# Performance work log

Measured on AMD Instinct MI355X. Metric: run time of the kernel, lower is better.

## Reference

```python
import jax, jax.numpy as jnp
import numpy as np

B, T, CH, V, E, L = 64, 1024, 256, 32000, 64, 128  # batch, enc_len, channel, vocab, emb_dim, latent_dims


def setup_inputs() -> dict:
    key = jax.random.key(0)
    ks = jax.random.split(key, 13)
    s = 0.05  # weight init scale
    return {
        "prev_cont_vec": jax.random.normal(ks[0], (B, CH), jnp.float32),
        "F": jax.random.normal(ks[1], (B, T, CH), jnp.float32),
        "prev_char": jax.random.normal(ks[2], (B, V), jnp.float32),
        "state_h": jax.random.normal(ks[3], (B, L), jnp.float32),
        "state_c": jax.random.normal(ks[4], (B, L), jnp.float32),
        # learned parameters (all Dense layers use_bias=False)
        "Wc": jax.random.normal(ks[5], (V, E), jnp.float32) * s,
        "Wct1": jax.random.normal(ks[6], (CH, E), jnp.float32) * s,
        "Wo": jax.random.normal(ks[7], (L, V), jnp.float32) * s,
        "Wct2": jax.random.normal(ks[8], (CH, V), jnp.float32) * s,
        "lstm_kernel": jax.random.normal(ks[9], (E, 4 * L), jnp.float32) * s,
        "lstm_recurrent": jax.random.normal(ks[10], (L, 4 * L), jnp.float32) * s,
        "W_h": jax.random.normal(ks[11], (L, CH), jnp.float32) * s,
        "V_attn": jax.random.normal(ks[12], (1, 1, CH), jnp.float32) * s,
    }


def reference(prev_cont_vec, F, prev_char, state_h, state_c,
              Wc, Wct1, Wo, Wct2, lstm_kernel, lstm_recurrent, W_h, V_attn):
    # lstm input: Wc(prev_char) + Wct1(prev_cont_vec)  -> [B, E]
    lstm_inp = prev_char @ Wc + prev_cont_vec @ Wct1
    # Keras LSTMCell (no bias), gate order i, f, c, o
    z = lstm_inp @ lstm_kernel + state_h @ lstm_recurrent  # [B, 4L]
    zi, zf, zg, zo = jnp.split(z, 4, axis=-1)
    i = jax.nn.sigmoid(zi)
    f = jax.nn.sigmoid(zf)
    g = jnp.tanh(zg)
    o = jax.nn.sigmoid(zo)
    new_c = f * state_c + i * g
    new_h = o * jnp.tanh(new_c)
    # training=True branch: clip returned cell state
    new_c_out = jnp.clip(new_c, -10.0, 10.0)
    # additive attention over time axis of F [B, T, CH]
    H_tfm = (new_h @ W_h)[:, None, :]            # [B, 1, CH]
    e_t = V_attn * jnp.tanh(H_tfm + F)           # [B, T, CH]
    attn = jax.nn.softmax(e_t, axis=1)           # softmax over T, per channel
    c_t = jnp.sum(attn * F, axis=1)              # [B, CH]
    # output distribution
    O_t = jax.nn.softmax(new_h @ Wo + c_t @ Wct2, axis=1)  # [B, V]
    return (O_t, c_t, new_h, new_c_out)
```

## Files before the change

kernel.cpp:

```cpp
#include <hip/hip_runtime.h>
#include <hip/hip_bf16.h>

#define BB 64
#define TT 1024
#define CHN 256
#define VV 32000
#define EE 64
#define LL 128
#define NC1 250
#define KC1 128
#define TS 8

typedef unsigned short u16;
typedef unsigned int u32;

__device__ __forceinline__ float fast_rcp(float x) { return __builtin_amdgcn_rcpf(x); }
__device__ __forceinline__ float tanh_fast(float y) {
    float e = __expf(2.0f * y);
    return 1.0f - 2.0f * fast_rcp(1.0f + e);
}
__device__ __forceinline__ float sigmoid_fast(float x) {
    return fast_rcp(1.0f + __expf(-x));
}

__global__ __launch_bounds__(256) void k1_stage1(const float* __restrict__ A,
                                                 const float* __restrict__ Wc,
                                                 float* __restrict__ part) {
    const int kc = blockIdx.x;
    const int k0 = kc * KC1;
    const int e  = threadIdx.x & 63;
    const int b0 = blockIdx.y * 32 + __builtin_amdgcn_readfirstlane(threadIdx.x >> 6) * 8;

    float acc[8];
    #pragma unroll
    for (int i = 0; i < 8; ++i) acc[i] = 0.0f;

    const float* W  = Wc + (size_t)k0 * EE + e;
    const float* Ar = A + (size_t)b0 * VV + k0;
    float wa[8], wb[8];
    #pragma unroll
    for (int j = 0; j < 8; ++j) wa[j] = W[(size_t)j * EE];

    for (int k = 0; k < KC1; k += 16) {
        #pragma unroll
        for (int j = 0; j < 8; ++j) wb[j] = W[(size_t)(k + 8 + j) * EE];
        #pragma unroll
        for (int j = 0; j < 8; ++j) {
            #pragma unroll
            for (int i = 0; i < 8; ++i)
                acc[i] = fmaf(Ar[(size_t)i * VV + k + j], wa[j], acc[i]);
        }
        if (k + 16 < KC1) {
            #pragma unroll
            for (int j = 0; j < 8; ++j) wa[j] = W[(size_t)(k + 16 + j) * EE];
        }
        #pragma unroll
        for (int j = 0; j < 8; ++j) {
            #pragma unroll
            for (int i = 0; i < 8; ++i)
                acc[i] = fmaf(Ar[(size_t)i * VV + k + 8 + j], wb[j], acc[i]);
        }
    }
    float* dst = part + (size_t)kc * (BB * EE) + b0 * EE + e;
    #pragma unroll
    for (int i = 0; i < 8; ++i) dst[i * EE] = acc[i];
}

__global__ __launch_bounds__(512) void k2_lstm(const float* __restrict__ part,
    const float* __restrict__ pcv, const float* __restrict__ state_h,
    const float* __restrict__ state_c, const float* __restrict__ Wct1,
    const float* __restrict__ lstm_kernel, const float* __restrict__ lstm_rec,
    const float* __restrict__ W_h,
    float* __restrict__ out_newh, float* __restrict__ out_newc,
    float* __restrict__ At, float* __restrict__ Htfm) {
    __shared__ float red[8][EE];
    __shared__ float inp[EE];
    __shared__ float sh[LL];
    __shared__ float z[4 * LL];
    __shared__ float nh[LL];
    const int b = blockIdx.x;
    const int t = threadIdx.x;
    const int e  = t & 63;
    const int g  = t >> 6;

    {
        float s = 0.0f;
        for (int j = g; j < NC1; j += 8)
            s += part[(size_t)j * (BB * EE) + b * EE + e];
        const int c0 = g * 32;
        #pragma unroll 8
        for (int c = 0; c < 32; ++c)
            s = fmaf(pcv[b * CHN + c0 + c], Wct1[(size_t)(c0 + c) * EE + e], s);
        red[g][e] = s;
    }
    __syncthreads();
    if (t < EE) {
        float s = 0.0f;
        #pragma unroll
        for (int j = 0; j < 8; ++j) s += red[j][t];
        inp[t] = s;
    } else if (t >= 64 && t < 64 + LL) {
        sh[t - 64] = state_h[b * LL + (t - 64)];
    }
    __syncthreads();
    {
        float a = 0.0f;
        #pragma unroll 8
        for (int e2 = 0; e2 < EE; ++e2) a = fmaf(inp[e2], lstm_kernel[e2 * 512 + t], a);
        #pragma unroll 8
        for (int l = 0; l < LL; ++l) a = fmaf(sh[l], lstm_rec[l * 512 + t], a);
        z[t] = a;
    }
    __syncthreads();
    if (t < LL) {
        float zi = z[t], zf = z[LL + t], zg = z[2 * LL + t], zo = z[3 * LL + t];
        float ig = sigmoid_fast(zi);
        float fg = sigmoid_fast(zf);
        float gg = tanh_fast(zg);
        float og = sigmoid_fast(zo);
        float co = state_c[b * LL + t];
        float cn = fg * co + ig * gg;
        float hn = og * tanh_fast(cn);
        out_newc[b * LL + t] = fminf(fmaxf(cn, -10.0f), 10.0f);
        out_newh[b * LL + t] = hn;
        At[t * BB + b] = hn;
        nh[t] = hn;
    }
    __syncthreads();
    if (t < CHN) {
        float a = 0.0f;
        #pragma unroll 8
        for (int l = 0; l < LL; ++l) a = fmaf(nh[l], W_h[l * CHN + t], a);
        Htfm[b * CHN + t] = a;
    }
}

__global__ __launch_bounds__(256) void k3_attn(const float* __restrict__ F,
    const float* __restrict__ Htfm, const float* __restrict__ Vattn,
    float* __restrict__ pS, float* __restrict__ pW) {
    __shared__ float4 sS[256];
    __shared__ float4 sW[256];
    const int b    = blockIdx.x;
    const int ts   = blockIdx.y;
    const int lane = threadIdx.x & 63;
    const int w    = threadIdx.x >> 6;
    const int ch   = lane * 4;

    float4 h = *(const float4*)(Htfm + b * CHN + ch);
    float4 v = *(const float4*)(Vattn + ch);
    float s0 = 0, s1 = 0, s2 = 0, s3 = 0;
    float a0 = 0, a1 = 0, a2 = 0, a3 = 0;

    const float* Fp = F + ((size_t)b * TT + ts * (TT / TS) + w * 32) * CHN + ch;
    #pragma unroll 4
    for (int t = 0; t < 32; ++t) {
        float4 f = *(const float4*)(Fp + (size_t)t * CHN);
        float e0 = __expf(v.x * tanh_fast(h.x + f.x));
        float e1 = __expf(v.y * tanh_fast(h.y + f.y));
        float e2 = __expf(v.z * tanh_fast(h.z + f.z));
        float e3 = __expf(v.w * tanh_fast(h.w + f.w));
        s0 += e0; s1 += e1; s2 += e2; s3 += e3;
        a0 = fmaf(e0, f.x, a0); a1 = fmaf(e1, f.y, a1);
        a2 = fmaf(e2, f.z, a2); a3 = fmaf(e3, f.w, a3);
    }
    sS[threadIdx.x] = make_float4(s0, s1, s2, s3);
    sW[threadIdx.x] = make_float4(a0, a1, a2, a3);
    __syncthreads();
    if (threadIdx.x < 64) {
        float4 S = sS[threadIdx.x];
        float4 W = sW[threadIdx.x];
        #pragma unroll
        for (int j = 1; j < 4; ++j) {
            float4 s = sS[j * 64 + threadIdx.x];
            float4 q = sW[j * 64 + threadIdx.x];
            S.x += s.x; S.y += s.y; S.z += s.z; S.w += s.w;
            W.x += q.x; W.y += q.y; W.z += q.z; W.w += q.w;
        }
        int base = (b * TS + ts) * CHN + threadIdx.x * 4;
        *(float4*)(pS + base) = S;
        *(float4*)(pW + base) = W;
    }
}

__global__ __launch_bounds__(256) void k4_combine(const float* __restrict__ pS,
    const float* __restrict__ pW, float* __restrict__ out_ct, float* __restrict__ At,
    float* __restrict__ rowsum) {
    const int b = blockIdx.x;
    const int ch = threadIdx.x;
    float S = 0.0f, W = 0.0f;
    #pragma unroll
    for (int j = 0; j < TS; ++j) {
        int idx = (b * TS + j) * CHN + ch;
        S += pS[idx];
        W += pW[idx];
    }
    float c = W / S;
    out_ct[b * CHN + ch] = c;
    At[(LL + ch) * BB + b] = c;
    if (b == 0 && ch < BB) rowsum[ch] = 0.0f;
}

__device__ __forceinline__ void k5_phase(const float* __restrict__ W, int kn,
    const float* __restrict__ Abase, float acc[8]) {
    float wa[8], wb[8];
    #pragma unroll
    for (int j = 0; j < 8; ++j) wa[j] = W[(size_t)j * VV];
    for (int k = 0; k < kn; k += 16) {
        #pragma unroll
        for (int j = 0; j < 8; ++j) wb[j] = W[(size_t)(k + 8 + j) * VV];
        #pragma unroll
        for (int j = 0; j < 8; ++j) {
            const float* a = Abase + (size_t)(k + j) * BB;
            #pragma unroll
            for (int i = 0; i < 8; ++i) acc[i] = fmaf(a[i], wa[j], acc[i]);
        }
        if (k + 16 < kn) {
            #pragma unroll
            for (int j = 0; j < 8; ++j) wa[j] = W[(size_t)(k + 16 + j) * VV];
        }
        #pragma unroll
        for (int j = 0; j < 8; ++j) {
            const float* a = Abase + (size_t)(k + 8 + j) * BB;
            #pragma unroll
            for (int i = 0; i < 8; ++i) acc[i] = fmaf(a[i], wb[j], acc[i]);
        }
    }
}

__global__ __launch_bounds__(256) void k5_logits(const float* __restrict__ Wo,
    const float* __restrict__ Wct2, const float* __restrict__ At,
    float* __restrict__ outO) {
    const int v  = blockIdx.x * 64 + (threadIdx.x & 63);
    const int b0 = blockIdx.y * 32 + __builtin_amdgcn_readfirstlane(threadIdx.x >> 6) * 8;
    float acc[8];
    #pragma unroll
    for (int i = 0; i < 8; ++i) acc[i] = 0.0f;

    k5_phase(Wo + v, LL, At + b0, acc);
    k5_phase(Wct2 + v, CHN, At + (size_t)LL * BB + b0, acc);

    #pragma unroll
    for (int i = 0; i < 8; ++i) outO[(size_t)(b0 + i) * VV + v] = acc[i];
}

__global__ __launch_bounds__(256) void k5b_expsum(const float* __restrict__ O,
                                                  float* __restrict__ rowsum) {
    __shared__ float red[256];
    const int b = blockIdx.x;
    const int c = blockIdx.y;
    const int t = threadIdx.x;
    const float4* row4 = (const float4*)(O + (size_t)b * VV);

    float s = 0.0f;
    for (int i = c * 2000 + t; i < (c + 1) * 2000; i += 256) {
        float4 f = row4[i];
        s += __expf(f.x) + __expf(f.y) + __expf(f.z) + __expf(f.w);
    }
    red[t] = s;
    __syncthreads();
    for (int off = 128; off > 0; off >>= 1) {
        if (t < off) red[t] += red[t + off];
        __syncthreads();
    }
    if (t == 0) atomicAdd(&rowsum[b], red[0]);
}

__global__ __launch_bounds__(256) void k5c_norm(float* __restrict__ O,
                                                const float* __restrict__ rowsum) {
    const int gid = blockIdx.x * 256 + threadIdx.x;
    float4* O4 = (float4*)O;
    const u32 row = ((u32)gid * 4u) / (u32)VV;
    const float inv = fast_rcp(rowsum[row]);
    float4 f = O4[gid];
    f.x = __expf(f.x) * inv;
    f.y = __expf(f.y) * inv;
    f.z = __expf(f.z) * inv;
    f.w = __expf(f.w) * inv;
    O4[gid] = f;
}

extern "C" void kernel_launch(void* const* d_in, const int* in_sizes, int n_in,
                              void* d_out, int out_size, void* d_ws, size_t ws_size,
                              hipStream_t stream) {
    (void)in_sizes; (void)n_in; (void)out_size; (void)ws_size;
    const float* pcv       = (const float*)d_in[0];
    const float* F         = (const float*)d_in[1];
    const float* prev_char = (const float*)d_in[2];
    const float* state_h   = (const float*)d_in[3];
    const float* state_c   = (const float*)d_in[4];
    const float* Wc        = (const float*)d_in[5];
    const float* Wct1      = (const float*)d_in[6];
    const float* Wo        = (const float*)d_in[7];
    const float* Wct2      = (const float*)d_in[8];
    const float* lstm_k    = (const float*)d_in[9];
    const float* lstm_r    = (const float*)d_in[10];
    const float* W_h       = (const float*)d_in[11];
    const float* Vattn     = (const float*)d_in[12];

    float* outO  = (float*)d_out;
    float* outCt = outO + (size_t)BB * VV;
    float* outH  = outCt + (size_t)BB * CHN;
    float* outC  = outH + (size_t)BB * LL;

    float* ws     = (float*)d_ws;
    float* part   = ws;
    float* pS     = part + (size_t)NC1 * BB * EE;
    float* pW     = pS + (size_t)BB * TS * CHN;
    float* At     = pW + (size_t)BB * TS * CHN;
    float* Htfm   = At + (LL + CHN) * BB;
    float* rowsum = part;

    hipLaunchKernelGGL(k1_stage1, dim3(NC1, 2), dim3(256), 0, stream, prev_char, Wc, part);
    hipLaunchKernelGGL(k2_lstm, dim3(BB), dim3(512), 0, stream, part, pcv, state_h,
                       state_c, Wct1, lstm_k, lstm_r, W_h, outH, outC, At, Htfm);
    hipLaunchKernelGGL(k3_attn, dim3(BB, TS), dim3(256), 0, stream, F, Htfm, Vattn, pS, pW);
    hipLaunchKernelGGL(k4_combine, dim3(BB), dim3(256), 0, stream, pS, pW, outCt, At, rowsum);
    hipLaunchKernelGGL(k5_logits, dim3(VV / 64, 2), dim3(256), 0, stream, Wo, Wct2, At, outO);
    hipLaunchKernelGGL(k5b_expsum, dim3(BB, 4), dim3(256), 0, stream, outO, rowsum);
    hipLaunchKernelGGL(k5c_norm, dim3((BB * VV / 4) / 256), dim3(256), 0, stream, outO, rowsum);
}
```

Before: 257.0 us.

## Stage GEMM operands in LDS, fuse exp into logits, split attention finer

The first-stage and logits kernels now load their activation and weight tiles into shared memory before computing. The logits kernel computes two vocab columns per thread and applies the exponential itself, so the later row-sum and normalize passes no longer recompute exp. The attention kernel doubles its time-axis split and prefetches the next F row. The partial-sum layout is transposed so each batch row's partials are contiguous for the LSTM kernel. This adds shared-memory use and barriers, and changes the workspace offsets.

```diff
diff --git a/kernel.cpp b/kernel.cpp
--- a/kernel.cpp
+++ b/kernel.cpp
@@ -9,7 +9,7 @@
 #define LL 128
 #define NC1 250
 #define KC1 128
-#define TS 8
+#define TS 16
 
 typedef unsigned short u16;
 typedef unsigned int u32;
@@ -26,44 +26,55 @@
 __global__ __launch_bounds__(256) void k1_stage1(const float* __restrict__ A,
                                                  const float* __restrict__ Wc,
                                                  float* __restrict__ part) {
+    __shared__ float sW[KC1][EE];
+    __shared__ float sAT[KC1][32];
     const int kc = blockIdx.x;
     const int k0 = kc * KC1;
-    const int e  = threadIdx.x & 63;
-    const int b0 = blockIdx.y * 32 + __builtin_amdgcn_readfirstlane(threadIdx.x >> 6) * 8;
-
+    const int y  = blockIdx.y;
+    const int t  = threadIdx.x;
+
+    #pragma unroll
+    for (int f = t; f < 2048; f += 256)
+        *(float4*)(&sW[0][0] + f * 4) = *(const float4*)(Wc + (size_t)k0 * EE + f * 4);
+    {
+        const int bl = t & 31;
+        const int kq = t >> 5;
+        const float* src = A + (size_t)(y * 32 + bl) * VV + k0 + kq * 16;
+        #pragma unroll
+        for (int j4 = 0; j4 < 4; ++j4) {
+            float4 v = *(const float4*)(src + j4 * 4);
+            sAT[kq * 16 + j4 * 4 + 0][bl] = v.x;
+            sAT[kq * 16 + j4 * 4 + 1][bl] = v.y;
+            sAT[kq * 16 + j4 * 4 + 2][bl] = v.z;
+            sAT[kq * 16 + j4 * 4 + 3][bl] = v.w;
+        }
+    }
+    __syncthreads();
+
+    const int e  = t & 63;
+    const int b0 = (t >> 6) * 8;
     float acc[8];
     #pragma unroll
     for (int i = 0; i < 8; ++i) acc[i] = 0.0f;
 
-    const float* W  = Wc + (size_t)k0 * EE + e;
-    const float* Ar = A + (size_t)b0 * VV + k0;
-    float wa[8], wb[8];
-    #pragma unroll
-    for (int j = 0; j < 8; ++j) wa[j] = W[(size_t)j * EE];
-
-    for (int k = 0; k < KC1; k += 16) {
-        #pragma unroll
-        for (int j = 0; j < 8; ++j) wb[j] = W[(size_t)(k + 8 + j) * EE];
-        #pragma unroll
-        for (int j = 0; j < 8; ++j) {
-            #pragma unroll
-            for (int i = 0; i < 8; ++i)
-                acc[i] = fmaf(Ar[(size_t)i * VV + k + j], wa[j], acc[i]);
-        }
-        if (k + 16 < KC1) {
-            #pragma unroll
-            for (int j = 0; j < 8; ++j) wa[j] = W[(size_t)(k + 16 + j) * EE];
-        }
-        #pragma unroll
-        for (int j = 0; j < 8; ++j) {
-            #pragma unroll
-            for (int i = 0; i < 8; ++i)
-                acc[i] = fmaf(Ar[(size_t)i * VV + k + 8 + j], wb[j], acc[i]);
-        }
-    }
-    float* dst = part + (size_t)kc * (BB * EE) + b0 * EE + e;
-    #pragma unroll
-    for (int i = 0; i < 8; ++i) dst[i * EE] = acc[i];
+    #pragma unroll 4
+    for (int k = 0; k < KC1; ++k) {
+        float wt = sW[k][e];
+        float4 a0 = *(const float4*)&sAT[k][b0];
+        float4 a1 = *(const float4*)&sAT[k][b0 + 4];
+        acc[0] = fmaf(a0.x, wt, acc[0]);
+        acc[1] = fmaf(a0.y, wt, acc[1]);
+        acc[2] = fmaf(a0.z, wt, acc[2]);
+        acc[3] = fmaf(a0.w, wt, acc[3]);
+        acc[4] = fmaf(a1.x, wt, acc[4]);
+        acc[5] = fmaf(a1.y, wt, acc[5]);
+        acc[6] = fmaf(a1.z, wt, acc[6]);
+        acc[7] = fmaf(a1.w, wt, acc[7]);
+    }
+    const int gb = y * 32 + b0;
+    #pragma unroll
+    for (int i = 0; i < 8; ++i)
+        part[((size_t)(gb + i) * NC1 + kc) * EE + e] = acc[i];
 }
 
 __global__ __launch_bounds__(512) void k2_lstm(const float* __restrict__ part,
@@ -86,7 +97,7 @@
     {
         float s = 0.0f;
         for (int j = g; j < NC1; j += 8)
-            s += part[(size_t)j * (BB * EE) + b * EE + e];
+            s += part[((size_t)b * NC1 + j) * EE + e];
         const int c0 = g * 32;
         #pragma unroll 8
         for (int c = 0; c < 32; ++c)
@@ -151,17 +162,20 @@
     float s0 = 0, s1 = 0, s2 = 0, s3 = 0;
     float a0 = 0, a1 = 0, a2 = 0, a3 = 0;
 
-    const float* Fp = F + ((size_t)b * TT + ts * (TT / TS) + w * 32) * CHN + ch;
-    #pragma unroll 4
-    for (int t = 0; t < 32; ++t) {
-        float4 f = *(const float4*)(Fp + (size_t)t * CHN);
-        float e0 = __expf(v.x * tanh_fast(h.x + f.x));
-        float e1 = __expf(v.y * tanh_fast(h.y + f.y));
-        float e2 = __expf(v.z * tanh_fast(h.z + f.z));
-        float e3 = __expf(v.w * tanh_fast(h.w + f.w));
+    const float* Fp = F + ((size_t)b * TT + ts * (TT / TS) + w * 16) * CHN + ch;
+    float4 cur = *(const float4*)(Fp);
+    #pragma unroll
+    for (int t = 0; t < 16; ++t) {
+        float4 nxt;
+        if (t < 15) nxt = *(const float4*)(Fp + (size_t)(t + 1) * CHN);
+        float e0 = __expf(v.x * tanh_fast(h.x + cur.x));
+        float e1 = __expf(v.y * tanh_fast(h.y + cur.y));
+        float e2 = __expf(v.z * tanh_fast(h.z + cur.z));
+        float e3 = __expf(v.w * tanh_fast(h.w + cur.w));
         s0 += e0; s1 += e1; s2 += e2; s3 += e3;
-        a0 = fmaf(e0, f.x, a0); a1 = fmaf(e1, f.y, a1);
-        a2 = fmaf(e2, f.z, a2); a3 = fmaf(e3, f.w, a3);
+        a0 = fmaf(e0, cur.x, a0); a1 = fmaf(e1, cur.y, a1);
+        a2 = fmaf(e2, cur.z, a2); a3 = fmaf(e3, cur.w, a3);
+        cur = nxt;
     }
     sS[threadIdx.x] = make_float4(s0, s1, s2, s3);
     sW[threadIdx.x] = make_float4(a0, a1, a2, a3);
@@ -201,28 +215,44 @@
 }
 
 __device__ __forceinline__ void k5_phase(const float* __restrict__ W, int kn,
-    const float* __restrict__ Abase, float acc[8]) {
-    float wa[8], wb[8];
-    #pragma unroll
-    for (int j = 0; j < 8; ++j) wa[j] = W[(size_t)j * VV];
-    for (int k = 0; k < kn; k += 16) {
-        #pragma unroll
-        for (int j = 0; j < 8; ++j) wb[j] = W[(size_t)(k + 8 + j) * VV];
-        #pragma unroll
-        for (int j = 0; j < 8; ++j) {
-            const float* a = Abase + (size_t)(k + j) * BB;
+    const float* sAt, float2 acc[8]) {
+    float2 wa[4], wb[4];
+    #pragma unroll
+    for (int j = 0; j < 4; ++j) wa[j] = *(const float2*)(W + (size_t)j * VV);
+    for (int k = 0; k < kn; k += 8) {
+        #pragma unroll
+        for (int j = 0; j < 4; ++j) wb[j] = *(const float2*)(W + (size_t)(k + 4 + j) * VV);
+        #pragma unroll
+        for (int j = 0; j < 4; ++j) {
+            const float* a = sAt + (size_t)(k + j) * 32;
+            float4 x = *(const float4*)a;
+            float4 z = *(const float4*)(a + 4);
+            acc[0].x = fmaf(x.x, wa[j].x, acc[0].x); acc[0].y = fmaf(x.x, wa[j].y, acc[0].y);
+            acc[1].x = fmaf(x.y, wa[j].x, acc[1].x); acc[1].y = fmaf(x.y, wa[j].y, acc[1].y);
+            acc[2].x = fmaf(x.z, wa[j].x, acc[2].x); acc[2].y = fmaf(x.z, wa[j].y, acc[2].y);
+            acc[3].x = fmaf(x.w, wa[j].x, acc[3].x); acc[3].y = fmaf(x.w, wa[j].y, acc[3].y);
+            acc[4].x = fmaf(z.x, wa[j].x, acc[4].x); acc[4].y = fmaf(z.x, wa[j].y, acc[4].y);
+            acc[5].x = fmaf(z.y, wa[j].x, acc[5].x); acc[5].y = fmaf(z.y, wa[j].y, acc[5].y);
+            acc[6].x = fmaf(z.z, wa[j].x, acc[6].x); acc[6].y = fmaf(z.z, wa[j].y, acc[6].y);
+            acc[7].x = fmaf(z.w, wa[j].x, acc[7].x); acc[7].y = fmaf(z.w, wa[j].y, acc[7].y);
+        }
+        if (k + 8 < kn) {
             #pragma unroll
-            for (int i = 0; i < 8; ++i) acc[i] = fmaf(a[i], wa[j], acc[i]);
-        }
-        if (k + 16 < kn) {
-            #pragma unroll
-            for (int j = 0; j < 8; ++j) wa[j] = W[(size_t)(k + 16 + j) * VV];
-        }
-        #pragma unroll
-        for (int j = 0; j < 8; ++j) {
-            const float* a = Abase + (size_t)(k + 8 + j) * BB;
-            #pragma unroll
-            for (int i = 0; i < 8; ++i) acc[i] = fmaf(a[i], wb[j], acc[i]);
+            for (int j = 0; j < 4; ++j) wa[j] = *(const float2*)(W + (size_t)(k + 8 + j) * VV);
+        }
+        #pragma unroll
+        for (int j = 0; j < 4; ++j) {
+            const float* a = sAt + (size_t)(k + 4 + j) * 32;
+            float4 x = *(const float4*)a;
+            float4 z = *(const float4*)(a + 4);
+            acc[0].x = fmaf(x.x, wb[j].x, acc[0].x); acc[0].y = fmaf(x.x, wb[j].y, acc[0].y);
+            acc[1].x = fmaf(x.y, wb[j].x, acc[1].x); acc[1].y = fmaf(x.y, wb[j].y, acc[1].y);
+            acc[2].x = fmaf(x.z, wb[j].x, acc[2].x); acc[2].y = fmaf(x.z, wb[j].y, acc[2].y);
+            acc[3].x = fmaf(x.w, wb[j].x, acc[3].x); acc[3].y = fmaf(x.w, wb[j].y, acc[3].y);
+            acc[4].x = fmaf(z.x, wb[j].x, acc[4].x); acc[4].y = fmaf(z.x, wb[j].y, acc[4].y);
+            acc[5].x = fmaf(z.y, wb[j].x, acc[5].x); acc[5].y = fmaf(z.y, wb[j].y, acc[5].y);
+            acc[6].x = fmaf(z.z, wb[j].x, acc[6].x); acc[6].y = fmaf(z.z, wb[j].y, acc[6].y);
+            acc[7].x = fmaf(z.w, wb[j].x, acc[7].x); acc[7].y = fmaf(z.w, wb[j].y, acc[7].y);
         }
     }
 }
@@ -230,17 +260,34 @@
 __global__ __launch_bounds__(256) void k5_logits(const float* __restrict__ Wo,
     const float* __restrict__ Wct2, const float* __restrict__ At,
     float* __restrict__ outO) {
-    const int v  = blockIdx.x * 64 + (threadIdx.x & 63);
-    const int b0 = blockIdx.y * 32 + __builtin_amdgcn_readfirstlane(threadIdx.x >> 6) * 8;
-    float acc[8];
-    #pragma unroll
-    for (int i = 0; i < 8; ++i) acc[i] = 0.0f;
-
-    k5_phase(Wo + v, LL, At + b0, acc);
-    k5_phase(Wct2 + v, CHN, At + (size_t)LL * BB + b0, acc);
-
-    #pragma unroll
-    for (int i = 0; i < 8; ++i) outO[(size_t)(b0 + i) * VV + v] = acc[i];
+    __shared__ float sAt[384][32];
+    const int y = blockIdx.y;
+    const int t = threadIdx.x;
+
+    #pragma unroll
+    for (int f = t; f < 3072; f += 256) {
+        int k  = f >> 3;
+        int c4 = (f & 7) * 4;
+        *(float4*)&sAt[k][c4] = *(const float4*)(At + (size_t)k * BB + y * 32 + c4);
+    }
+    __syncthreads();
+
+    const int lane = t & 63;
+    const int v2   = blockIdx.x * 128 + lane * 2;
+    const int w8   = (t >> 6) * 8;
+    float2 acc[8];
+    #pragma unroll
+    for (int i = 0; i < 8; ++i) acc[i] = make_float2(0.0f, 0.0f);
+
+    k5_phase(Wo + v2, LL, &sAt[0][0] + w8, acc);
+    k5_phase(Wct2 + v2, CHN, &sAt[LL][0] + w8, acc);
+
+    const int gb = y * 32 + w8;
+    #pragma unroll
+    for (int i = 0; i < 8; ++i) {
+        float2 ex = make_float2(__expf(acc[i].x), __expf(acc[i].y));
+        *(float2*)(outO + (size_t)(gb + i) * VV + v2) = ex;
+    }
 }
 
 __global__ __launch_bounds__(256) void k5b_expsum(const float* __restrict__ O,
@@ -254,7 +301,7 @@
     float s = 0.0f;
     for (int i = c * 2000 + t; i < (c + 1) * 2000; i += 256) {
         float4 f = row4[i];
-        s += __expf(f.x) + __expf(f.y) + __expf(f.z) + __expf(f.w);
+        s += f.x + f.y + f.z + f.w;
     }
     red[t] = s;
     __syncthreads();
@@ -272,10 +319,7 @@
     const u32 row = ((u32)gid * 4u) / (u32)VV;
     const float inv = fast_rcp(rowsum[row]);
     float4 f = O4[gid];
-    f.x = __expf(f.x) * inv;
-    f.y = __expf(f.y) * inv;
-    f.z = __expf(f.z) * inv;
-    f.w = __expf(f.w) * inv;
+    f.x *= inv; f.y *= inv; f.z *= inv; f.w *= inv;
     O4[gid] = f;
 }
 
@@ -315,7 +359,7 @@
                        state_c, Wct1, lstm_k, lstm_r, W_h, outH, outC, At, Htfm);
     hipLaunchKernelGGL(k3_attn, dim3(BB, TS), dim3(256), 0, stream, F, Htfm, Vattn, pS, pW);
     hipLaunchKernelGGL(k4_combine, dim3(BB), dim3(256), 0, stream, pS, pW, outCt, At, rowsum);
-    hipLaunchKernelGGL(k5_logits, dim3(VV / 64, 2), dim3(256), 0, stream, Wo, Wct2, At, outO);
+    hipLaunchKernelGGL(k5_logits, dim3(NC1, 2), dim3(256), 0, stream, Wo, Wct2, At, outO);
     hipLaunchKernelGGL(k5b_expsum, dim3(BB, 4), dim3(256), 0, stream, outO, rowsum);
     hipLaunchKernelGGL(k5c_norm, dim3((BB * VV / 4) / 256), dim3(256), 0, stream, outO, rowsum);
 }
```

Measured after the change: 251.3 us. 2.2% less time.
